# Kernel optimization log

Measured on AMD Instinct MI355X. Metric: run time of the kernel, lower is better.

## Reference

```python
import jax, jax.numpy as jnp
import numpy as np

EPS = 1e-5
B, F, C, H, L, S = 8192, 128, 256, 512, 4, 10


def _gelu(x):
    return jax.nn.gelu(x, approximate=False)  # torch nn.GELU default = exact erf


def _ln(x, g, b):
    m = jnp.mean(x, axis=-1, keepdims=True)
    v = jnp.var(x, axis=-1, keepdims=True)  # biased, matches torch LayerNorm
    return (x - m) / jnp.sqrt(v + EPS) * g + b


def setup_inputs() -> dict:
    key = jax.random.key(0)
    ks = iter(jax.random.split(key, 40))

    def w(shape, fan_in):
        return jax.random.normal(next(ks), shape, jnp.float32) / np.float32(np.sqrt(fan_in))

    def z0(*s):
        return jnp.zeros(s, jnp.float32)

    return dict(
        x=jax.random.normal(next(ks), (B, F), jnp.float32),
        context=jax.random.normal(next(ks), (B, C), jnp.float32),
        u=jax.random.normal(next(ks), (S, B, F), jnp.float32),
        Wi=w((F, H), F), bi=z0(H),
        Wt1=w((1, H), 1), bt1=z0(H), Wt2=w((H, H), H), bt2=z0(H),
        Wc1=w((C, 2 * H), C), bc1=z0(2 * H), Wc2=w((2 * H, H), 2 * H), bc2=z0(H),
        Wv=w((L, H, H), H), bv=z0(L, H), Woa=w((L, H, H), H), boa=z0(L, H),
        g1=jnp.ones((L, H), jnp.float32), be1=z0(L, H),
        Wm1=w((L, H, 4 * H), H), bm1=z0(L, 4 * H),
        Wm2=w((L, 4 * H, H), 4 * H), bm2=z0(L, H),
        g2=jnp.ones((L, H), jnp.float32), be2=z0(L, H),
        Wcv=w((L, H, H), H), bcv=z0(L, H), Wco=w((L, H, H), H), bco=z0(L, H),
        scale=0.5 * jnp.ones((L,), jnp.float32),
        Wp1=w((H, H), H), bp1=z0(H), Wp2=w((H, F), H), bp2=z0(F),
    )


def _forward(x, context, u, Wi, bi, Wt1, bt1, Wt2, bt2, Wc1, bc1, Wc2, bc2,
             Wv, bv, Woa, boa, g1, be1, Wm1, bm1, Wm2, bm2, g2, be2,
             Wcv, bcv, Wco, bco, scale, Wp1, bp1, Wp2, bp2):
    n_steps = u.shape[0]
    dt = 1.0 / n_steps
    nb = x.shape[0]
    nl = Wv.shape[0]

    # context projection, computed once as in torch
    ctx = _gelu(context @ Wc1 + bc1) @ Wc2 + bc2  # [B,H]
    # seq_len==1 cross-attention: softmax over a single key == 1, so the output
    # is out_proj(v_proj(ctx)) and does not depend on x -> precompute per layer.
    vctx = jnp.einsum('bh,lhk->lbk', ctx, Wcv) + bcv[:, None, :]    # [L,B,H]
    xatt = jnp.einsum('lbh,lhk->lbk', vctx, Wco) + bco[:, None, :]  # [L,B,H]

    def vel(z, t):
        tt = jnp.clip(t, 0.0, 1.0)[:, None]                          # [B,1]
        h = z @ Wi + bi + (_gelu(tt @ Wt1 + bt1) @ Wt2 + bt2)        # [B,H]
        for l in range(nl):
            # seq_len==1 self-attention collapses to out_proj(v_proj(h))
            attn = (h @ Wv[l] + bv[l]) @ Woa[l] + boa[l]
            h = _ln(h + attn, g1[l], be1[l])
            mlp = _gelu(h @ Wm1[l] + bm1[l]) @ Wm2[l] + bm2[l]
            h = _ln(h + mlp, g2[l], be2[l])
            h = h + scale[l] * xatt[l]
        return _gelu(h @ Wp1 + bp1) @ Wp2 + bp2                      # [B,F]

    def step(carry, inp):
        z, ld = carry
        t_val, u_k = inp
        t = jnp.full((nb,), t_val, jnp.float32)
        zs = jax.lax.stop_gradient(z)  # matches z.detach()/leaf z_req in torch
        v, Ju = jax.jvp(lambda zz: vel(zz, t), (zs,), (u_k,))
        ld = ld + jnp.sum(u_k * Ju, axis=-1) * dt  # Hutchinson u^T J u
        return (zs + v * dt, ld), None

    ts = jnp.arange(n_steps, dtype=jnp.float32) * dt
    (z, log_det), _ = jax.lax.scan(step, (x, jnp.zeros((nb,), jnp.float32)), (ts, u))
    return z, log_det


def reference(x, context, u, Wi, bi, Wt1, bt1, Wt2, bt2, Wc1, bc1, Wc2, bc2,
              Wv, bv, Woa, boa, g1, be1, Wm1, bm1, Wm2, bm2, g2, be2,
              Wcv, bcv, Wco, bco, scale, Wp1, bp1, Wp2, bp2):
    return _forward(x, context, u, Wi, bi, Wt1, bt1, Wt2, bt2, Wc1, bc1, Wc2, bc2,
                    Wv, bv, Woa, boa, g1, be1, Wm1, bm1, Wm2, bm2, g2, be2,
                    Wcv, bcv, Wco, bco, scale, Wp1, bp1, Wp2, bp2)
```

## Files before the change

kernel.cpp:

```cpp
#include <hip/hip_runtime.h>
#include <math.h>

using floatx16 = __attribute__((ext_vector_type(16))) float;
using bf16x8   = __attribute__((ext_vector_type(8))) __bf16;
using ushort8  = __attribute__((ext_vector_type(8))) unsigned short;

__device__ __forceinline__ float b2f(unsigned short u) {
  unsigned v = ((unsigned)u) << 16; float f; __builtin_memcpy(&f, &v, 4); return f;
}
__device__ __forceinline__ unsigned short f2b(float f) {
  unsigned u; __builtin_memcpy(&u, &f, 4);
  u += 0x7fffu + ((u >> 16) & 1u);
  return (unsigned short)(u >> 16);
}
__device__ __forceinline__ float gelu_f(float x) {
  return 0.5f * x * (1.0f + erff(x * 0.7071067811865475f));
}
__device__ __forceinline__ floatx16 zero16() {
  floatx16 z;
  #pragma unroll
  for (int e = 0; e < 16; e++) z[e] = 0.f;
  return z;
}

#define SWZS(r, c) (((r) << 5) + ((((c) ^ ((r) & 3))) << 3))

template<int MODE>
__global__ __launch_bounds__(256) void gemm_bt_k(
    const unsigned short* __restrict__ A, const unsigned short* __restrict__ Bt,
    void* __restrict__ C, const float* __restrict__ bias,
    const float* __restrict__ bias2, int M, int N, int K)
{
  __shared__ unsigned short As[2 * 128 * 32];
  __shared__ unsigned short Bs[2 * 128 * 32];
  const int tid  = threadIdx.x;
  const int lane = tid & 63;
  const int wave = tid >> 6;

  int bx = blockIdx.x, by = blockIdx.y;
  if ((gridDim.y & 7) == 0) {
    int lin = by * gridDim.x + bx;
    int xcd = lin & 7;
    int w   = lin >> 3;
    by = xcd * (gridDim.y >> 3) + w / gridDim.x;
    bx = w % gridDim.x;
  }
  const int row0 = by * 128;
  const int col0 = bx * 128;

  const int r0 = lane >> 2;
  const int cj = lane & 3;
  const unsigned short* Ag = A  + (size_t)(row0 + wave * 32 + r0) * K + cj * 8;
  const unsigned short* Bg = Bt + (size_t)(col0 + wave * 32 + r0) * K + cj * 8;
  const int aw0 = SWZS(wave * 32 + r0, cj);

  const int wr = wave >> 1, wc = wave & 1;
  const int m32 = lane & 31;
  const int hi  = lane >> 5;

  floatx16 acc[2][2];
  acc[0][0] = zero16(); acc[0][1] = zero16();
  acc[1][0] = zero16(); acc[1][1] = zero16();

  ushort8 ra0, ra1, rb0, rb1;
  ra0 = *(const ushort8*)(Ag);
  ra1 = *(const ushort8*)(Ag + (size_t)16 * K);
  rb0 = *(const ushort8*)(Bg);
  rb1 = *(const ushort8*)(Bg + (size_t)16 * K);

  int p = 0;
  for (int k0 = 0; k0 < K; k0 += 32) {
    unsigned short* Ab = &As[p * 4096];
    unsigned short* Bb = &Bs[p * 4096];
    *(ushort8*)(Ab + aw0)            = ra0;
    *(ushort8*)(Ab + aw0 + 16 * 32)  = ra1;
    *(ushort8*)(Bb + aw0)            = rb0;
    *(ushort8*)(Bb + aw0 + 16 * 32)  = rb1;
    __syncthreads();
    if (k0 + 32 < K) {
      ra0 = *(const ushort8*)(Ag + k0 + 32);
      ra1 = *(const ushort8*)(Ag + (size_t)16 * K + k0 + 32);
      rb0 = *(const ushort8*)(Bg + k0 + 32);
      rb1 = *(const ushort8*)(Bg + (size_t)16 * K + k0 + 32);
    }
    bf16x8 af[2][2], bfr[2][2];
    #pragma unroll
    for (int i = 0; i < 2; i++)
      #pragma unroll
      for (int h = 0; h < 2; h++)
        af[i][h] = *(const bf16x8*)&Ab[SWZS(wr * 64 + i * 32 + m32, 2 * h + hi)];
    #pragma unroll
    for (int j = 0; j < 2; j++)
      #pragma unroll
      for (int h = 0; h < 2; h++)
        bfr[j][h] = *(const bf16x8*)&Bb[SWZS(wc * 64 + j * 32 + m32, 2 * h + hi)];
    #pragma unroll
    for (int h = 0; h < 2; h++)
      #pragma unroll
      for (int i = 0; i < 2; i++)
        #pragma unroll
        for (int j = 0; j < 2; j++)
          acc[i][j] = __builtin_amdgcn_mfma_f32_32x32x16_bf16(af[i][h], bfr[j][h], acc[i][j], 0, 0, 0);
    p ^= 1;
  }

  #pragma unroll
  for (int j = 0; j < 2; j++) {
    int col = col0 + wc * 64 + j * 32 + m32;
    float bb = bias ? bias[col] : 0.f;
    if (MODE >= 2) { if (bias2) bb += bias2[col]; }
    #pragma unroll
    for (int i = 0; i < 2; i++) {
      int rb = row0 + wr * 64 + i * 32 + 4 * hi;
      if (MODE == 3) {
        #pragma unroll
        for (int pr = 0; pr < 8; pr++) {
          int re = rb + 2 * (pr & 1) + 8 * (pr >> 1);
          float pv = acc[i][j][2 * pr] + bb;
          float tv = acc[i][j][2 * pr + 1];
          float cdf = 0.5f * (1.0f + erff(pv * 0.7071067811865475f));
          float pdf = 0.3989422804014327f * expf(-0.5f * pv * pv);
          ((unsigned short*)C)[(size_t)re * N + col]       = f2b(pv * cdf);
          ((unsigned short*)C)[(size_t)(re + 1) * N + col] = f2b((cdf + pv * pdf) * tv);
        }
      } else {
        #pragma unroll
        for (int reg = 0; reg < 16; reg++) {
          int row = rb + (reg & 3) + 8 * (reg >> 2);
          float v = acc[i][j][reg];
          if (MODE == 0 || MODE == 1) v += bb;
          if (MODE == 2) { if ((reg & 1) == 0) v += bb; }
          if (MODE == 1) v = gelu_f(v);
          ((unsigned short*)C)[(size_t)row * N + col] = f2b(v);
        }
      }
    }
  }
}

template<bool XATT>
__global__ __launch_bounds__(256) void gemm_ln_k(
    const unsigned short* __restrict__ A, const unsigned short* __restrict__ Bt,
    unsigned short* __restrict__ h, const float* __restrict__ bias,
    const float* __restrict__ g, const float* __restrict__ be,
    const unsigned short* __restrict__ xatt, const float* __restrict__ sc_p,
    int K)
{
  constexpr int N = 512;
  __shared__ unsigned short As[2 * 64 * 32];
  __shared__ unsigned short Bs[2 * 512 * 32];
  __shared__ float red[32][2][4];
  const int tid = threadIdx.x, lane = tid & 63, wave = tid >> 6;
  const int row0 = blockIdx.x * 64;

  const int r0 = lane >> 2;
  const int cj = lane & 3;
  const unsigned short* Ag = A + (size_t)(row0 + wave * 16 + r0) * K + cj * 8;
  const int awA = SWZS(wave * 16 + r0, cj);
  const unsigned short* Bg = Bt + (size_t)(wave * 128 + r0) * K + cj * 8;
  const int bwr = wave * 128 + r0;

  const int wr = wave >> 1, wc = wave & 1;
  const int m32 = lane & 31;
  const int hi  = lane >> 5;

  floatx16 acc[8];
  #pragma unroll
  for (int j = 0; j < 8; j++) acc[j] = zero16();

  ushort8 ra0, rbv[8];
  ra0 = *(const ushort8*)(Ag);
  #pragma unroll
  for (int t = 0; t < 8; t++)
    rbv[t] = *(const ushort8*)(Bg + (size_t)16 * t * K);

  int p = 0;
  for (int k0 = 0; k0 < K; k0 += 32) {
    unsigned short* Ab = &As[p * 2048];
    unsigned short* Bb = &Bs[p * 16384];
    *(ushort8*)&Ab[awA] = ra0;
    #pragma unroll
    for (int t = 0; t < 8; t++)
      *(ushort8*)&Bb[SWZS(bwr + 16 * t, cj)] = rbv[t];
    __syncthreads();
    if (k0 + 32 < K) {
      ra0 = *(const ushort8*)(Ag + k0 + 32);
      #pragma unroll
      for (int t = 0; t < 8; t++)
        rbv[t] = *(const ushort8*)(Bg + (size_t)16 * t * K + k0 + 32);
    }
    bf16x8 af[2], bfr[8][2];
    #pragma unroll
    for (int hh = 0; hh < 2; hh++)
      af[hh] = *(const bf16x8*)&Ab[SWZS(wr * 32 + m32, 2 * hh + hi)];
    #pragma unroll
    for (int j = 0; j < 8; j++)
      #pragma unroll
      for (int hh = 0; hh < 2; hh++)
        bfr[j][hh] = *(const bf16x8*)&Bs[p * 16384 + SWZS(wc * 256 + j * 32 + m32, 2 * hh + hi)];
    #pragma unroll
    for (int hh = 0; hh < 2; hh++)
      #pragma unroll
      for (int j = 0; j < 8; j++)
        acc[j] = __builtin_amdgcn_mfma_f32_32x32x16_bf16(af[hh], bfr[j][hh], acc[j], 0, 0, 0);
    p ^= 1;
  }

  float bc[8], gc[8], bec[8];
  #pragma unroll
  for (int j = 0; j < 8; j++) {
    int col = wc * 256 + j * 32 + m32;
    bc[j] = bias[col]; gc[j] = g[col]; bec[j] = be[col];
  }

  #pragma unroll
  for (int pr = 0; pr < 8; pr++) {
    int re = wr * 32 + 4 * hi + 2 * (pr & 1) + 8 * (pr >> 1);
    size_t ge = (size_t)(row0 + re) * N;
    float sx = 0.f, sxx = 0.f, sdv = 0.f, sxdv = 0.f;
    #pragma unroll
    for (int j = 0; j < 8; j++) {
      int col = wc * 256 + j * 32 + m32;
      float xp = acc[j][2 * pr]     + bc[j] + b2f(h[ge + col]);
      float dv = acc[j][2 * pr + 1]         + b2f(h[ge + N + col]);
      acc[j][2 * pr] = xp; acc[j][2 * pr + 1] = dv;
      sx += xp; sxx += xp * xp; sdv += dv; sxdv += xp * dv;
    }
    #pragma unroll
    for (int off = 1; off <= 16; off <<= 1) {
      sx   += __shfl_xor(sx, off, 64);
      sxx  += __shfl_xor(sxx, off, 64);
      sdv  += __shfl_xor(sdv, off, 64);
      sxdv += __shfl_xor(sxdv, off, 64);
    }
    if (m32 == 0) {
      int pid = re >> 1;
      red[pid][wc][0] = sx; red[pid][wc][1] = sxx;
      red[pid][wc][2] = sdv; red[pid][wc][3] = sxdv;
    }
  }
  __syncthreads();

  const float inv = 1.0f / 512.0f;
  float sl = 0.f;
  if (XATT) sl = *sc_p;
  #pragma unroll
  for (int pr = 0; pr < 8; pr++) {
    int re = wr * 32 + 4 * hi + 2 * (pr & 1) + 8 * (pr >> 1);
    int pid = re >> 1;
    float sx   = red[pid][0][0] + red[pid][1][0];
    float sxx  = red[pid][0][1] + red[pid][1][1];
    float sdv  = red[pid][0][2] + red[pid][1][2];
    float sxdv = red[pid][0][3] + red[pid][1][3];
    float m = sx * inv;
    float var = sxx * inv - m * m;
    float rstd = rsqrtf(var + 1e-5f);
    float dm = sdv * inv;
    float cm = (sxdv - m * sdv) * inv * rstd;
    size_t ge = (size_t)(row0 + re) * N;
    size_t bx_ = (size_t)((row0 + re) >> 1) * N;
    #pragma unroll
    for (int j = 0; j < 8; j++) {
      int col = wc * 256 + j * 32 + m32;
      float xp = acc[j][2 * pr], dv = acc[j][2 * pr + 1];
      float xh = (xp - m) * rstd;
      float y = xh * gc[j] + bec[j];
      if (XATT) y += sl * b2f(xatt[bx_ + col]);
      float dy = gc[j] * rstd * (dv - dm - xh * cm);
      h[ge + col]     = f2b(y);
      h[ge + N + col] = f2b(dy);
    }
  }
}

__global__ __launch_bounds__(256, 2) void gemm_wide3_k(
    const unsigned short* __restrict__ A, const unsigned short* __restrict__ Bt,
    unsigned short* __restrict__ C, const float* __restrict__ bias,
    int M, int N, int K)
{
  __shared__ unsigned short As[2 * 128 * 32];
  __shared__ unsigned short Bs[2 * 256 * 32];
  const int tid  = threadIdx.x;
  const int lane = tid & 63;
  const int wave = tid >> 6;

  int bx = blockIdx.x, by = blockIdx.y;
  if ((gridDim.y & 7) == 0) {
    int lin = by * gridDim.x + bx;
    int xcd = lin & 7;
    int w   = lin >> 3;
    by = xcd * (gridDim.y >> 3) + w / gridDim.x;
    bx = w % gridDim.x;
  }
  const int row0 = by * 128;
  const int col0 = bx * 256;

  const int r0 = lane >> 2;
  const int cj = lane & 3;
  const unsigned short* Ag = A  + (size_t)(row0 + wave * 32 + r0) * K + cj * 8;
  const unsigned short* Bg = Bt + (size_t)(col0 + wave * 64 + r0) * K + cj * 8;
  const int awr = wave * 32 + r0;
  const int bwr = wave * 64 + r0;

  const int wr = wave >> 1, wc = wave & 1;
  const int m32 = lane & 31;
  const int hi  = lane >> 5;

  floatx16 acc[2][4];
  #pragma unroll
  for (int i = 0; i < 2; i++)
    #pragma unroll
    for (int j = 0; j < 4; j++) acc[i][j] = zero16();

  ushort8 ra0, ra1, rbv[4];
  ra0 = *(const ushort8*)(Ag);
  ra1 = *(const ushort8*)(Ag + (size_t)16 * K);
  #pragma unroll
  for (int t = 0; t < 4; t++)
    rbv[t] = *(const ushort8*)(Bg + (size_t)16 * t * K);

  int p = 0;
  for (int k0 = 0; k0 < K; k0 += 32) {
    unsigned short* Ab = &As[p * 4096];
    unsigned short* Bb = &Bs[p * 8192];
    *(ushort8*)&Ab[SWZS(awr, cj)]      = ra0;
    *(ushort8*)&Ab[SWZS(awr + 16, cj)] = ra1;
    #pragma unroll
    for (int t = 0; t < 4; t++)
      *(ushort8*)&Bb[SWZS(bwr + 16 * t, cj)] = rbv[t];
    __syncthreads();
    if (k0 + 32 < K) {
      ra0 = *(const ushort8*)(Ag + k0 + 32);
      ra1 = *(const ushort8*)(Ag + (size_t)16 * K + k0 + 32);
      #pragma unroll
      for (int t = 0; t < 4; t++)
        rbv[t] = *(const ushort8*)(Bg + (size_t)16 * t * K + k0 + 32);
    }
    bf16x8 af[2][2], bfr[4][2];
    #pragma unroll
    for (int i = 0; i < 2; i++)
      #pragma unroll
      for (int h = 0; h < 2; h++)
        af[i][h] = *(const bf16x8*)&Ab[SWZS(wr * 64 + i * 32 + m32, 2 * h + hi)];
    #pragma unroll
    for (int j = 0; j < 4; j++)
      #pragma unroll
      for (int h = 0; h < 2; h++)
        bfr[j][h] = *(const bf16x8*)&Bb[SWZS(wc * 128 + j * 32 + m32, 2 * h + hi)];
    #pragma unroll
    for (int h = 0; h < 2; h++)
      #pragma unroll
      for (int i = 0; i < 2; i++)
        #pragma unroll
        for (int j = 0; j < 4; j++)
          acc[i][j] = __builtin_amdgcn_mfma_f32_32x32x16_bf16(af[i][h], bfr[j][h], acc[i][j], 0, 0, 0);
    p ^= 1;
  }

  #pragma unroll
  for (int j = 0; j < 4; j++) {
    int col = col0 + wc * 128 + j * 32 + m32;
    float bb = bias[col];
    #pragma unroll
    for (int i = 0; i < 2; i++) {
      int rb = row0 + wr * 64 + i * 32 + 4 * hi;
      #pragma unroll
      for (int pr = 0; pr < 8; pr++) {
        int re = rb + 2 * (pr & 1) + 8 * (pr >> 1);
        float pv = acc[i][j][2 * pr] + bb;
        float tv = acc[i][j][2 * pr + 1];
        float cdf = 0.5f * (1.0f + erff(pv * 0.7071067811865475f));
        float pdf = 0.3989422804014327f * expf(-0.5f * pv * pv);
        C[(size_t)re * N + col]       = f2b(pv * cdf);
        C[(size_t)(re + 1) * N + col] = f2b((cdf + pv * pdf) * tv);
      }
    }
  }
}

__global__ __launch_bounds__(256) void gemm_vout_k(
    const unsigned short* __restrict__ A, const unsigned short* __restrict__ Bt,
    const float* __restrict__ bias, const float* __restrict__ u_cur,
    const float* __restrict__ u_next, float* __restrict__ zf,
    float* __restrict__ ldb, unsigned short* __restrict__ Abuf,
    int K, float dtv)
{
  constexpr int N = 128;
  __shared__ unsigned short As[2 * 128 * 32];
  __shared__ unsigned short Bs[2 * 128 * 32];
  __shared__ float red[64][2];
  const int tid = threadIdx.x, lane = tid & 63, wave = tid >> 6;
  const int row0 = blockIdx.x * 128;

  const int r0 = lane >> 2;
  const int cj = lane & 3;
  const unsigned short* Ag = A  + (size_t)(row0 + wave * 32 + r0) * K + cj * 8;
  const unsigned short* Bg = Bt + (size_t)(wave * 32 + r0) * K + cj * 8;
  const int aw0 = SWZS(wave * 32 + r0, cj);

  const int wr = wave >> 1, wc = wave & 1;
  const int m32 = lane & 31;
  const int hi  = lane >> 5;

  floatx16 acc[2][2];
  acc[0][0] = zero16(); acc[0][1] = zero16();
  acc[1][0] = zero16(); acc[1][1] = zero16();

  ushort8 ra0, ra1, rb0, rb1;
  ra0 = *(const ushort8*)(Ag);
  ra1 = *(const ushort8*)(Ag + (size_t)16 * K);
  rb0 = *(const ushort8*)(Bg);
  rb1 = *(const ushort8*)(Bg + (size_t)16 * K);

  int p = 0;
  for (int k0 = 0; k0 < K; k0 += 32) {
    unsigned short* Ab = &As[p * 4096];
    unsigned short* Bb = &Bs[p * 4096];
    *(ushort8*)(Ab + aw0)           = ra0;
    *(ushort8*)(Ab + aw0 + 16 * 32) = ra1;
    *(ushort8*)(Bb + aw0)           = rb0;
    *(ushort8*)(Bb + aw0 + 16 * 32) = rb1;
    __syncthreads();
    if (k0 + 32 < K) {
      ra0 = *(const ushort8*)(Ag + k0 + 32);
      ra1 = *(const ushort8*)(Ag + (size_t)16 * K + k0 + 32);
      rb0 = *(const ushort8*)(Bg + k0 + 32);
      rb1 = *(const ushort8*)(Bg + (size_t)16 * K + k0 + 32);
    }
    bf16x8 af[2][2], bfr[2][2];
    #pragma unroll
    for (int i = 0; i < 2; i++)
      #pragma unroll
      for (int h = 0; h < 2; h++)
        af[i][h] = *(const bf16x8*)&Ab[SWZS(wr * 64 + i * 32 + m32, 2 * h + hi)];
    #pragma unroll
    for (int j = 0; j < 2; j++)
      #pragma unroll
      for (int h = 0; h < 2; h++)
        bfr[j][h] = *(const bf16x8*)&Bb[SWZS(wc * 64 + j * 32 + m32, 2 * h + hi)];
    #pragma unroll
    for (int h = 0; h < 2; h++)
      #pragma unroll
      for (int i = 0; i < 2; i++)
        #pragma unroll
        for (int j = 0; j < 2; j++)
          acc[i][j] = __builtin_amdgcn_mfma_f32_32x32x16_bf16(af[i][h], bfr[j][h], acc[i][j], 0, 0, 0);
    p ^= 1;
  }

  #pragma unroll
  for (int i = 0; i < 2; i++) {
    #pragma unroll
    for (int pr = 0; pr < 8; pr++) {
      int re_loc = wr * 64 + i * 32 + 4 * hi + 2 * (pr & 1) + 8 * (pr >> 1);
      size_t growe = (size_t)(row0 + re_loc);
      size_t b = growe >> 1;
      float dacc = 0.f;
      #pragma unroll
      for (int j = 0; j < 2; j++) {
        int col = wc * 64 + j * 32 + m32;
        float v  = acc[i][j][2 * pr] + bias[col];
        float Ju = acc[i][j][2 * pr + 1];
        float z = zf[b * N + col] + v * dtv;
        zf[b * N + col] = z;
        Abuf[growe * N + col] = f2b(z);
        if (u_next) Abuf[(growe + 1) * N + col] = f2b(u_next[b * N + col]);
        dacc += u_cur[b * N + col] * Ju;
      }
      #pragma unroll
      for (int off = 1; off <= 16; off <<= 1) dacc += __shfl_xor(dacc, off, 64);
      if (m32 == 0) red[re_loc >> 1][wc] = dacc;
    }
  }
  __syncthreads();
  if (tid < 64) ldb[(row0 >> 1) + tid] += (red[tid][0] + red[tid][1]) * dtv;
}

__global__ void transpose_cast_k(const float* __restrict__ W,
                                 unsigned short* __restrict__ Wt, int K, int N)
{
  __shared__ float tile[32][33];
  size_t off = (size_t)blockIdx.z * K * N;
  const float* Wp = W + off;
  unsigned short* Wtp = Wt + off;
  int bx = blockIdx.x, by = blockIdx.y;
  int tx = threadIdx.x, ty = threadIdx.y;
  #pragma unroll
  for (int i = ty; i < 32; i += 8)
    tile[i][tx] = Wp[(size_t)(by * 32 + i) * N + bx * 32 + tx];
  __syncthreads();
  #pragma unroll
  for (int i = ty; i < 32; i += 8)
    Wtp[(size_t)(bx * 32 + i) * K + by * 32 + tx] = f2b(tile[tx][i]);
}

__global__ __launch_bounds__(256) void zero_k(float* __restrict__ p, int n) {
  int i = (int)(blockIdx.x * blockDim.x + threadIdx.x);
  if (i < n) p[i] = 0.f;
}

__global__ __launch_bounds__(256) void combine_bias_k(
    const float* __restrict__ bvp, const float* __restrict__ Wb,
    const float* __restrict__ bo, float* __restrict__ bout, int H)
{
  int out = blockIdx.x * blockDim.x + threadIdx.x;
  int l   = blockIdx.y;
  int kc  = blockIdx.z;
  const float* A2 = Wb + (size_t)l * H * H;
  float s = (kc == 0) ? bo[(size_t)l * H + out] : 0.f;
  int kend = (kc + 1) * 64;
  for (int k = kc * 64; k < kend; k++) s += bvp[(size_t)l * H + k] * A2[(size_t)k * H + out];
  atomicAdd(&bout[(size_t)l * H + out], s);
}

__global__ __launch_bounds__(256) void cast_k(const float* __restrict__ in,
                                              unsigned short* __restrict__ out, size_t n) {
  size_t i = blockIdx.x * blockDim.x + threadIdx.x;
  if (i < n) out[i] = f2b(in[i]);
}

__global__ __launch_bounds__(512) void temb_all_k(
    const float* __restrict__ Wt1, const float* __restrict__ bt1,
    const float* __restrict__ Wt2, const float* __restrict__ bt2,
    float dtv, float* __restrict__ tvecs, int H)
{
  __shared__ float e[512];
  int j = threadIdx.x;
  float t = fminf(fmaxf((float)blockIdx.x * dtv, 0.f), 1.f);
  e[j] = gelu_f(t * Wt1[j] + bt1[j]);
  __syncthreads();
  float s = bt2[j];
  for (int k = 0; k < H; k++) s += e[k] * Wt2[(size_t)k * H + j];
  tvecs[(size_t)blockIdx.x * H + j] = s;
}

__global__ __launch_bounds__(256) void init_k(
    const float* __restrict__ x, const float* __restrict__ u0,
    float* __restrict__ zf, float* __restrict__ ld,
    unsigned short* __restrict__ Abuf, int BF, int Bsz, int F)
{
  int i = (int)(blockIdx.x * blockDim.x + threadIdx.x);
  if (i < BF) {
    int r = i / F, c = i - r * F;
    float v = x[i];
    zf[i] = v;
    Abuf[(size_t)(2 * r) * F + c]     = f2b(v);
    Abuf[(size_t)(2 * r + 1) * F + c] = f2b(u0[i]);
  }
  if (i < Bsz) ld[i] = 0.f;
}

__global__ __launch_bounds__(256) void final_k(
    const float* __restrict__ zf, const float* __restrict__ ld,
    float* __restrict__ out, int BF, int Bsz)
{
  int i = (int)(blockIdx.x * blockDim.x + threadIdx.x);
  if (i < BF) out[i] = zf[i];
  if (i < Bsz) out[BF + i] = ld[i];
}

extern "C" void kernel_launch(void* const* d_in, const int* in_sizes, int n_in,
                              void* d_out, int out_size, void* d_ws, size_t ws_size,
                              hipStream_t stream) {
  constexpr int B = 8192, F = 128, C = 256, H = 512, L = 4, S = 10;
  constexpr int B2 = 2 * B;
  constexpr int BF = B * F;
  const float dtv = 1.0f / S;

  const float* x    = (const float*)d_in[0];
  const float* ctxI = (const float*)d_in[1];
  const float* u    = (const float*)d_in[2];
  const float* Wi   = (const float*)d_in[3];
  const float* bi   = (const float*)d_in[4];
  const float* Wt1  = (const float*)d_in[5];
  const float* bt1  = (const float*)d_in[6];
  const float* Wt2  = (const float*)d_in[7];
  const float* bt2  = (const float*)d_in[8];
  const float* Wc1  = (const float*)d_in[9];
  const float* bc1  = (const float*)d_in[10];
  const float* Wc2  = (const float*)d_in[11];
  const float* bc2  = (const float*)d_in[12];
  const float* Wv   = (const float*)d_in[13];
  const float* bv   = (const float*)d_in[14];
  const float* Woa  = (const float*)d_in[15];
  const float* boa  = (const float*)d_in[16];
  const float* g1   = (const float*)d_in[17];
  const float* be1  = (const float*)d_in[18];
  const float* Wm1  = (const float*)d_in[19];
  const float* bm1  = (const float*)d_in[20];
  const float* Wm2  = (const float*)d_in[21];
  const float* bm2  = (const float*)d_in[22];
  const float* g2   = (const float*)d_in[23];
  const float* be2  = (const float*)d_in[24];
  const float* Wcv  = (const float*)d_in[25];
  const float* bcv  = (const float*)d_in[26];
  const float* Wco  = (const float*)d_in[27];
  const float* bco  = (const float*)d_in[28];
  const float* scal = (const float*)d_in[29];
  const float* Wp1  = (const float*)d_in[30];
  const float* bp1  = (const float*)d_in[31];
  const float* Wp2  = (const float*)d_in[32];
  const float* bp2  = (const float*)d_in[33];

  char* wp = (char*)d_ws;
  auto alloc = [&](size_t bytes) -> void* {
    void* r = (void*)wp;
    wp += (bytes + 255) & ~(size_t)255;
    return r;
  };
  unsigned short* wWit  = (unsigned short*)alloc((size_t)H * F * 2);
  unsigned short* wWc1t = (unsigned short*)alloc((size_t)2 * H * C * 2);
  unsigned short* wWc2t = (unsigned short*)alloc((size_t)H * 2 * H * 2);
  unsigned short* wWvoT = (unsigned short*)alloc((size_t)L * H * H * 2);
  unsigned short* wCtxT = (unsigned short*)alloc((size_t)L * H * H * 2);
  unsigned short* wWm1t = (unsigned short*)alloc((size_t)L * 4 * H * H * 2);
  unsigned short* wWm2t = (unsigned short*)alloc((size_t)L * H * 4 * H * 2);
  unsigned short* wWp1t = (unsigned short*)alloc((size_t)H * H * 2);
  unsigned short* wWp2t = (unsigned short*)alloc((size_t)F * H * 2);
  unsigned short* wOaT  = (unsigned short*)alloc((size_t)L * H * H * 2);
  unsigned short* wCoT  = (unsigned short*)alloc((size_t)L * H * H * 2);
  unsigned short* wVb   = (unsigned short*)alloc((size_t)L * H * H * 2);
  unsigned short* wCvb  = (unsigned short*)alloc((size_t)L * H * H * 2);
  float* bcomb          = (float*)alloc((size_t)2 * L * H * 4);
  float* bvo  = bcomb;
  float* cbvo = bcomb + (size_t)L * H;
  float* tvecs          = (float*)alloc((size_t)S * H * 4);
  unsigned short* ctxc  = (unsigned short*)alloc((size_t)B * C * 2);
  unsigned short* Abuf  = (unsigned short*)alloc((size_t)B2 * F * 2);
  unsigned short* hbuf  = (unsigned short*)alloc((size_t)B2 * H * 2);
  unsigned short* tmp2  = (unsigned short*)alloc((size_t)B2 * H * 2);
  unsigned short* mbuf  = (unsigned short*)alloc((size_t)B2 * 4 * H * 2);
  unsigned short* xattb = (unsigned short*)alloc((size_t)L * B * H * 2);
  float* zf             = (float*)alloc((size_t)B * F * 4);
  float* ldb            = (float*)alloc((size_t)B * 4);
  (void)ws_size; (void)in_sizes; (void)n_in; (void)out_size;

  auto T = [&](const float* W, unsigned short* Wt, int K, int N, int Lz) {
    dim3 g(N / 32, K / 32, Lz);
    transpose_cast_k<<<g, dim3(32, 8), 0, stream>>>(W, Wt, K, N);
  };
  auto G = [&](int mode, const unsigned short* A, const unsigned short* Bt, void* Cc,
               const float* bias, const float* bias2, int M, int N, int K) {
    dim3 g(N / 128, M / 128);
    switch (mode) {
      case 0: gemm_bt_k<0><<<g, 256, 0, stream>>>(A, Bt, Cc, bias, bias2, M, N, K); break;
      case 1: gemm_bt_k<1><<<g, 256, 0, stream>>>(A, Bt, Cc, bias, bias2, M, N, K); break;
      case 2: gemm_bt_k<2><<<g, 256, 0, stream>>>(A, Bt, Cc, bias, bias2, M, N, K); break;
      case 3: gemm_bt_k<3><<<g, 256, 0, stream>>>(A, Bt, Cc, bias, bias2, M, N, K); break;
    }
  };

  T(Wi,  wWit,  F, H, 1);
  T(Wc1, wWc1t, C, 2 * H, 1);
  T(Wc2, wWc2t, 2 * H, H, 1);
  T(Wm1, wWm1t, H, 4 * H, L);
  T(Wm2, wWm2t, 4 * H, H, L);
  T(Wp1, wWp1t, H, H, 1);
  T(Wp2, wWp2t, H, F, 1);
  T(Woa, wOaT, H, H, L);
  T(Wco, wCoT, H, H, L);
  cast_k<<<((size_t)L * H * H + 255) / 256, 256, 0, stream>>>(Wv,  wVb,  (size_t)L * H * H);
  cast_k<<<((size_t)L * H * H + 255) / 256, 256, 0, stream>>>(Wcv, wCvb, (size_t)L * H * H);
  for (int l = 0; l < L; l++) {
    size_t o2 = (size_t)l * H * H;
    G(0, wOaT + o2, wVb  + o2, wWvoT + o2, nullptr, nullptr, H, H, H);
    G(0, wCoT + o2, wCvb + o2, wCtxT + o2, nullptr, nullptr, H, H, H);
  }
  zero_k<<<(2 * L * H + 255) / 256, 256, 0, stream>>>(bcomb, 2 * L * H);
  combine_bias_k<<<dim3(H / 256, L, H / 64), 256, 0, stream>>>(bv,  Woa, boa, bvo,  H);
  combine_bias_k<<<dim3(H / 256, L, H / 64), 256, 0, stream>>>(bcv, Wco, bco, cbvo, H);

  cast_k<<<(B * C + 255) / 256, 256, 0, stream>>>(ctxI, ctxc, (size_t)B * C);
  G(1, ctxc, wWc1t, mbuf, bc1, nullptr, B, 2 * H, C);
  G(0, mbuf, wWc2t, tmp2, bc2, nullptr, B, H, 2 * H);
  for (int l = 0; l < L; l++)
    G(0, tmp2, wCtxT + (size_t)l * H * H, xattb + (size_t)l * B * H,
      cbvo + l * H, nullptr, B, H, H);

  temb_all_k<<<S, H, 0, stream>>>(Wt1, bt1, Wt2, bt2, dtv, tvecs, H);
  init_k<<<(BF + 255) / 256, 256, 0, stream>>>(x, u, zf, ldb, Abuf, BF, B, F);

  for (int s = 0; s < S; s++) {
    G(2, Abuf, wWit, hbuf, bi, tvecs + (size_t)s * H, B2, H, F);
    for (int l = 0; l < L; l++) {
      size_t o2 = (size_t)l * H * H;
      size_t om = (size_t)l * 4 * H * H;
      gemm_ln_k<false><<<B2 / 64, 256, 0, stream>>>(
          hbuf, wWvoT + o2, hbuf, bvo + l * H, g1 + l * H, be1 + l * H,
          nullptr, nullptr, H);
      gemm_wide3_k<<<dim3(4 * H / 256, B2 / 128), 256, 0, stream>>>(
          hbuf, wWm1t + om, mbuf, bm1 + (size_t)l * 4 * H, B2, 4 * H, H);
      gemm_ln_k<true><<<B2 / 64, 256, 0, stream>>>(
          mbuf, wWm2t + om, hbuf, bm2 + l * H, g2 + l * H, be2 + l * H,
          xattb + (size_t)l * B * H, scal + l, 4 * H);
    }
    G(3, hbuf, wWp1t, tmp2, bp1, nullptr, B2, H, H);
    const float* u_cur = u + (size_t)s * BF;
    const float* u_next = (s + 1 < S) ? u + (size_t)(s + 1) * BF : nullptr;
    gemm_vout_k<<<B2 / 128, 256, 0, stream>>>(
        tmp2, wWp2t, bp2, u_cur, u_next, zf, ldb, Abuf, H, dtv);
  }

  final_k<<<(BF + 255) / 256, 256, 0, stream>>>(zf, ldb, (float*)d_out, BF, B);
}
```

Baseline: 7.797 ms.

## Use 8 waves per block in LN and wide GEMM kernels

The fused GEMM+LayerNorm kernel and the wide GELU GEMM now run with 512 threads (8 waves) per block instead of 4, keeping the same block tiles. Each wave now computes a smaller sub-tile with fewer accumulators, and global-to-LDS staging and the LN cross-wave reduction are redistributed to match. The aim is to cut per-thread register pressure and add more waves to hide latency. The cost is more waves contending for LDS and barriers per block, and in the LN kernel half the lanes of each wave sit idle while A is staged.

```diff
diff --git a/kernel.cpp b/kernel.cpp
--- a/kernel.cpp
+++ b/kernel.cpp
@@ -139,7 +139,7 @@
 }
 
 template<bool XATT>
-__global__ __launch_bounds__(256) void gemm_ln_k(
+__global__ __launch_bounds__(512, 4) void gemm_ln_k(
     const unsigned short* __restrict__ A, const unsigned short* __restrict__ Bt,
     unsigned short* __restrict__ h, const float* __restrict__ bias,
     const float* __restrict__ g, const float* __restrict__ be,
@@ -149,78 +149,79 @@
   constexpr int N = 512;
   __shared__ unsigned short As[2 * 64 * 32];
   __shared__ unsigned short Bs[2 * 512 * 32];
-  __shared__ float red[32][2][4];
+  __shared__ float red[32][4][4];
   const int tid = threadIdx.x, lane = tid & 63, wave = tid >> 6;
   const int row0 = blockIdx.x * 64;
 
   const int r0 = lane >> 2;
   const int cj = lane & 3;
-  const unsigned short* Ag = A + (size_t)(row0 + wave * 16 + r0) * K + cj * 8;
-  const int awA = SWZS(wave * 16 + r0, cj);
-  const unsigned short* Bg = Bt + (size_t)(wave * 128 + r0) * K + cj * 8;
-  const int bwr = wave * 128 + r0;
-
-  const int wr = wave >> 1, wc = wave & 1;
+  const int sa = wave * 8 + (r0 & 7);
+  const unsigned short* Ag = A + (size_t)(row0 + sa) * K + cj * 8;
+  const int awA = SWZS(sa, cj);
+  const unsigned short* Bg = Bt + (size_t)(wave * 64 + r0) * K + cj * 8;
+  const int bwr = wave * 64 + r0;
+
+  const int wr2 = wave >> 2, wc4 = wave & 3;
   const int m32 = lane & 31;
   const int hi  = lane >> 5;
 
-  floatx16 acc[8];
-  #pragma unroll
-  for (int j = 0; j < 8; j++) acc[j] = zero16();
-
-  ushort8 ra0, rbv[8];
-  ra0 = *(const ushort8*)(Ag);
-  #pragma unroll
-  for (int t = 0; t < 8; t++)
+  floatx16 acc[4];
+  #pragma unroll
+  for (int j = 0; j < 4; j++) acc[j] = zero16();
+
+  ushort8 ra, rbv[4];
+  if (lane < 32) ra = *(const ushort8*)(Ag);
+  #pragma unroll
+  for (int t = 0; t < 4; t++)
     rbv[t] = *(const ushort8*)(Bg + (size_t)16 * t * K);
 
   int p = 0;
   for (int k0 = 0; k0 < K; k0 += 32) {
     unsigned short* Ab = &As[p * 2048];
     unsigned short* Bb = &Bs[p * 16384];
-    *(ushort8*)&Ab[awA] = ra0;
-    #pragma unroll
-    for (int t = 0; t < 8; t++)
+    if (lane < 32) *(ushort8*)&Ab[awA] = ra;
+    #pragma unroll
+    for (int t = 0; t < 4; t++)
       *(ushort8*)&Bb[SWZS(bwr + 16 * t, cj)] = rbv[t];
     __syncthreads();
     if (k0 + 32 < K) {
-      ra0 = *(const ushort8*)(Ag + k0 + 32);
-      #pragma unroll
-      for (int t = 0; t < 8; t++)
+      if (lane < 32) ra = *(const ushort8*)(Ag + k0 + 32);
+      #pragma unroll
+      for (int t = 0; t < 4; t++)
         rbv[t] = *(const ushort8*)(Bg + (size_t)16 * t * K + k0 + 32);
     }
-    bf16x8 af[2], bfr[8][2];
+    bf16x8 af[2], bfr[4][2];
     #pragma unroll
     for (int hh = 0; hh < 2; hh++)
-      af[hh] = *(const bf16x8*)&Ab[SWZS(wr * 32 + m32, 2 * hh + hi)];
-    #pragma unroll
-    for (int j = 0; j < 8; j++)
+      af[hh] = *(const bf16x8*)&Ab[SWZS(wr2 * 32 + m32, 2 * hh + hi)];
+    #pragma unroll
+    for (int j = 0; j < 4; j++)
       #pragma unroll
       for (int hh = 0; hh < 2; hh++)
-        bfr[j][hh] = *(const bf16x8*)&Bs[p * 16384 + SWZS(wc * 256 + j * 32 + m32, 2 * hh + hi)];
+        bfr[j][hh] = *(const bf16x8*)&Bb[SWZS(wc4 * 128 + j * 32 + m32, 2 * hh + hi)];
     #pragma unroll
     for (int hh = 0; hh < 2; hh++)
       #pragma unroll
-      for (int j = 0; j < 8; j++)
+      for (int j = 0; j < 4; j++)
         acc[j] = __builtin_amdgcn_mfma_f32_32x32x16_bf16(af[hh], bfr[j][hh], acc[j], 0, 0, 0);
     p ^= 1;
   }
 
-  float bc[8], gc[8], bec[8];
-  #pragma unroll
-  for (int j = 0; j < 8; j++) {
-    int col = wc * 256 + j * 32 + m32;
+  float bc[4], gc[4], bec[4];
+  #pragma unroll
+  for (int j = 0; j < 4; j++) {
+    int col = wc4 * 128 + j * 32 + m32;
     bc[j] = bias[col]; gc[j] = g[col]; bec[j] = be[col];
   }
 
   #pragma unroll
   for (int pr = 0; pr < 8; pr++) {
-    int re = wr * 32 + 4 * hi + 2 * (pr & 1) + 8 * (pr >> 1);
+    int re = wr2 * 32 + 4 * hi + 2 * (pr & 1) + 8 * (pr >> 1);
     size_t ge = (size_t)(row0 + re) * N;
     float sx = 0.f, sxx = 0.f, sdv = 0.f, sxdv = 0.f;
     #pragma unroll
-    for (int j = 0; j < 8; j++) {
-      int col = wc * 256 + j * 32 + m32;
+    for (int j = 0; j < 4; j++) {
+      int col = wc4 * 128 + j * 32 + m32;
       float xp = acc[j][2 * pr]     + bc[j] + b2f(h[ge + col]);
       float dv = acc[j][2 * pr + 1]         + b2f(h[ge + N + col]);
       acc[j][2 * pr] = xp; acc[j][2 * pr + 1] = dv;
@@ -235,8 +236,8 @@
     }
     if (m32 == 0) {
       int pid = re >> 1;
-      red[pid][wc][0] = sx; red[pid][wc][1] = sxx;
-      red[pid][wc][2] = sdv; red[pid][wc][3] = sxdv;
+      red[pid][wc4][0] = sx; red[pid][wc4][1] = sxx;
+      red[pid][wc4][2] = sdv; red[pid][wc4][3] = sxdv;
     }
   }
   __syncthreads();
@@ -246,12 +247,12 @@
   if (XATT) sl = *sc_p;
   #pragma unroll
   for (int pr = 0; pr < 8; pr++) {
-    int re = wr * 32 + 4 * hi + 2 * (pr & 1) + 8 * (pr >> 1);
+    int re = wr2 * 32 + 4 * hi + 2 * (pr & 1) + 8 * (pr >> 1);
     int pid = re >> 1;
-    float sx   = red[pid][0][0] + red[pid][1][0];
-    float sxx  = red[pid][0][1] + red[pid][1][1];
-    float sdv  = red[pid][0][2] + red[pid][1][2];
-    float sxdv = red[pid][0][3] + red[pid][1][3];
+    float sx   = red[pid][0][0] + red[pid][1][0] + red[pid][2][0] + red[pid][3][0];
+    float sxx  = red[pid][0][1] + red[pid][1][1] + red[pid][2][1] + red[pid][3][1];
+    float sdv  = red[pid][0][2] + red[pid][1][2] + red[pid][2][2] + red[pid][3][2];
+    float sxdv = red[pid][0][3] + red[pid][1][3] + red[pid][2][3] + red[pid][3][3];
     float m = sx * inv;
     float var = sxx * inv - m * m;
     float rstd = rsqrtf(var + 1e-5f);
@@ -260,8 +261,8 @@
     size_t ge = (size_t)(row0 + re) * N;
     size_t bx_ = (size_t)((row0 + re) >> 1) * N;
     #pragma unroll
-    for (int j = 0; j < 8; j++) {
-      int col = wc * 256 + j * 32 + m32;
+    for (int j = 0; j < 4; j++) {
+      int col = wc4 * 128 + j * 32 + m32;
       float xp = acc[j][2 * pr], dv = acc[j][2 * pr + 1];
       float xh = (xp - m) * rstd;
       float y = xh * gc[j] + bec[j];
@@ -273,7 +274,7 @@
   }
 }
 
-__global__ __launch_bounds__(256, 2) void gemm_wide3_k(
+__global__ __launch_bounds__(512, 4) void gemm_wide3_k(
     const unsigned short* __restrict__ A, const unsigned short* __restrict__ Bt,
     unsigned short* __restrict__ C, const float* __restrict__ bias,
     int M, int N, int K)
@@ -297,83 +298,68 @@
 
   const int r0 = lane >> 2;
   const int cj = lane & 3;
-  const unsigned short* Ag = A  + (size_t)(row0 + wave * 32 + r0) * K + cj * 8;
-  const unsigned short* Bg = Bt + (size_t)(col0 + wave * 64 + r0) * K + cj * 8;
-  const int awr = wave * 32 + r0;
-  const int bwr = wave * 64 + r0;
-
-  const int wr = wave >> 1, wc = wave & 1;
+  const unsigned short* Ag = A  + (size_t)(row0 + wave * 16 + r0) * K + cj * 8;
+  const int awA = SWZS(wave * 16 + r0, cj);
+  const unsigned short* Bg = Bt + (size_t)(col0 + wave * 32 + r0) * K + cj * 8;
+  const int bwr = wave * 32 + r0;
+
+  const int wr4 = wave >> 1, wc2 = wave & 1;
   const int m32 = lane & 31;
   const int hi  = lane >> 5;
 
-  floatx16 acc[2][4];
-  #pragma unroll
-  for (int i = 0; i < 2; i++)
-    #pragma unroll
-    for (int j = 0; j < 4; j++) acc[i][j] = zero16();
-
-  ushort8 ra0, ra1, rbv[4];
-  ra0 = *(const ushort8*)(Ag);
-  ra1 = *(const ushort8*)(Ag + (size_t)16 * K);
-  #pragma unroll
-  for (int t = 0; t < 4; t++)
-    rbv[t] = *(const ushort8*)(Bg + (size_t)16 * t * K);
+  floatx16 acc[4];
+  #pragma unroll
+  for (int j = 0; j < 4; j++) acc[j] = zero16();
+
+  ushort8 ra, rbv[2];
+  ra = *(const ushort8*)(Ag);
+  rbv[0] = *(const ushort8*)(Bg);
+  rbv[1] = *(const ushort8*)(Bg + (size_t)16 * K);
 
   int p = 0;
   for (int k0 = 0; k0 < K; k0 += 32) {
     unsigned short* Ab = &As[p * 4096];
     unsigned short* Bb = &Bs[p * 8192];
-    *(ushort8*)&Ab[SWZS(awr, cj)]      = ra0;
-    *(ushort8*)&Ab[SWZS(awr + 16, cj)] = ra1;
-    #pragma unroll
-    for (int t = 0; t < 4; t++)
-      *(ushort8*)&Bb[SWZS(bwr + 16 * t, cj)] = rbv[t];
+    *(ushort8*)&Ab[awA] = ra;
+    *(ushort8*)&Bb[SWZS(bwr, cj)]      = rbv[0];
+    *(ushort8*)&Bb[SWZS(bwr + 16, cj)] = rbv[1];
     __syncthreads();
     if (k0 + 32 < K) {
-      ra0 = *(const ushort8*)(Ag + k0 + 32);
-      ra1 = *(const ushort8*)(Ag + (size_t)16 * K + k0 + 32);
-      #pragma unroll
-      for (int t = 0; t < 4; t++)
-        rbv[t] = *(const ushort8*)(Bg + (size_t)16 * t * K + k0 + 32);
-    }
-    bf16x8 af[2][2], bfr[4][2];
-    #pragma unroll
-    for (int i = 0; i < 2; i++)
-      #pragma unroll
-      for (int h = 0; h < 2; h++)
-        af[i][h] = *(const bf16x8*)&Ab[SWZS(wr * 64 + i * 32 + m32, 2 * h + hi)];
+      ra = *(const ushort8*)(Ag + k0 + 32);
+      rbv[0] = *(const ushort8*)(Bg + k0 + 32);
+      rbv[1] = *(const ushort8*)(Bg + (size_t)16 * K + k0 + 32);
+    }
+    bf16x8 af[2], bfr[4][2];
+    #pragma unroll
+    for (int hh = 0; hh < 2; hh++)
+      af[hh] = *(const bf16x8*)&Ab[SWZS(wr4 * 32 + m32, 2 * hh + hi)];
     #pragma unroll
     for (int j = 0; j < 4; j++)
       #pragma unroll
-      for (int h = 0; h < 2; h++)
-        bfr[j][h] = *(const bf16x8*)&Bb[SWZS(wc * 128 + j * 32 + m32, 2 * h + hi)];
-    #pragma unroll
-    for (int h = 0; h < 2; h++)
-      #pragma unroll
-      for (int i = 0; i < 2; i++)
-        #pragma unroll
-        for (int j = 0; j < 4; j++)
-          acc[i][j] = __builtin_amdgcn_mfma_f32_32x32x16_bf16(af[i][h], bfr[j][h], acc[i][j], 0, 0, 0);
+      for (int hh = 0; hh < 2; hh++)
+        bfr[j][hh] = *(const bf16x8*)&Bb[SWZS(wc2 * 128 + j * 32 + m32, 2 * hh + hi)];
+    #pragma unroll
+    for (int hh = 0; hh < 2; hh++)
+      #pragma unroll
+      for (int j = 0; j < 4; j++)
+        acc[j] = __builtin_amdgcn_mfma_f32_32x32x16_bf16(af[hh], bfr[j][hh], acc[j], 0, 0, 0);
     p ^= 1;
   }
 
   #pragma unroll
   for (int j = 0; j < 4; j++) {
-    int col = col0 + wc * 128 + j * 32 + m32;
+    int col = col0 + wc2 * 128 + j * 32 + m32;
     float bb = bias[col];
-    #pragma unroll
-    for (int i = 0; i < 2; i++) {
-      int rb = row0 + wr * 64 + i * 32 + 4 * hi;
-      #pragma unroll
-      for (int pr = 0; pr < 8; pr++) {
-        int re = rb + 2 * (pr & 1) + 8 * (pr >> 1);
-        float pv = acc[i][j][2 * pr] + bb;
-        float tv = acc[i][j][2 * pr + 1];
-        float cdf = 0.5f * (1.0f + erff(pv * 0.7071067811865475f));
-        float pdf = 0.3989422804014327f * expf(-0.5f * pv * pv);
-        C[(size_t)re * N + col]       = f2b(pv * cdf);
-        C[(size_t)(re + 1) * N + col] = f2b((cdf + pv * pdf) * tv);
-      }
+    int rb = row0 + wr4 * 32 + 4 * hi;
+    #pragma unroll
+    for (int pr = 0; pr < 8; pr++) {
+      int re = rb + 2 * (pr & 1) + 8 * (pr >> 1);
+      float pv = acc[j][2 * pr] + bb;
+      float tv = acc[j][2 * pr + 1];
+      float cdf = 0.5f * (1.0f + erff(pv * 0.7071067811865475f));
+      float pdf = 0.3989422804014327f * expf(-0.5f * pv * pv);
+      C[(size_t)re * N + col]       = f2b(pv * cdf);
+      C[(size_t)(re + 1) * N + col] = f2b((cdf + pv * pdf) * tv);
     }
   }
 }
@@ -685,12 +671,12 @@
     for (int l = 0; l < L; l++) {
       size_t o2 = (size_t)l * H * H;
       size_t om = (size_t)l * 4 * H * H;
-      gemm_ln_k<false><<<B2 / 64, 256, 0, stream>>>(
+      gemm_ln_k<false><<<B2 / 64, 512, 0, stream>>>(
           hbuf, wWvoT + o2, hbuf, bvo + l * H, g1 + l * H, be1 + l * H,
           nullptr, nullptr, H);
-      gemm_wide3_k<<<dim3(4 * H / 256, B2 / 128), 256, 0, stream>>>(
+      gemm_wide3_k<<<dim3(4 * H / 256, B2 / 128), 512, 0, stream>>>(
           hbuf, wWm1t + om, mbuf, bm1 + (size_t)l * 4 * H, B2, 4 * H, H);
-      gemm_ln_k<true><<<B2 / 64, 256, 0, stream>>>(
+      gemm_ln_k<true><<<B2 / 64, 512, 0, stream>>>(
           mbuf, wWm2t + om, hbuf, bm2 + l * H, g2 + l * H, be2 + l * H,
           xattb + (size_t)l * B * H, scal + l, 4 * H);
     }
```

After: 8.026 ms. +2.9%, slower.
